# Kernel optimization log

Hardware: AMD Instinct MI355X
Metric: run time of the kernel (lower is better)

The kernel has to match this reference:

```python
import jax, jax.numpy as jnp
import numpy as np

T, OBS, H, NOBJ = 32768, 256, 512, 4


def _xavier(key, shape):
    fan_in, fan_out = shape[0], shape[1]
    lim = jnp.sqrt(6.0 / (fan_in + fan_out)).astype(jnp.float32)
    return jax.random.uniform(key, shape, jnp.float32, -lim, lim)


def setup_inputs() -> dict:
    key = jax.random.key(0)
    ks = jax.random.split(key, 16)
    # weights stored as [in, out] so y = x @ W (same math as nn.Linear with W.T)
    return {
        "x": jax.random.normal(ks[0], (T, OBS), jnp.float32),
        "W_in0": _xavier(ks[1], (OBS, H)),
        "W_B0": _xavier(ks[2], (OBS, H)),
        "W_C0": _xavier(ks[3], (OBS, H)),
        "W_d0": _xavier(ks[4], (OBS, H)),
        "A_log0": jax.random.normal(ks[5], (H,), jnp.float32),
        "W_in1": _xavier(ks[6], (H, H)),
        "W_B1": _xavier(ks[7], (H, H)),
        "W_C1": _xavier(ks[8], (H, H)),
        "W_d1": _xavier(ks[9], (H, H)),
        "A_log1": jax.random.normal(ks[10], (H,), jnp.float32),
        "W_out": _xavier(ks[11], (H, NOBJ)),
        "b_out": jnp.zeros((NOBJ,), jnp.float32),
        "W_skip": _xavier(ks[12], (OBS, NOBJ)),
    }


def _mamba_layer(x, W_in, W_B, W_C, W_d, A_log):
    # x: [T, D_in] -> [T, H]
    x_state = x @ W_in           # [T, H]
    B = x @ W_B                  # [T, H]
    C = x @ W_C                  # [T, H]
    delta = jax.nn.sigmoid(x @ W_d)  # [T, H]
    A = -jnp.exp(A_log)          # [H]
    A_bar = jnp.exp(delta * A)   # [T, H], in (0, 1)
    Bx = B * x_state             # [T, H]

    def step(h, inp):
        a_t, bx_t = inp
        h = a_t * h + bx_t
        return h, h

    h0 = jnp.zeros((x_state.shape[-1],), x_state.dtype)
    _, h_seq = jax.lax.scan(step, h0, (A_bar, Bx))  # [T, H]
    return C * h_seq


def reference(x, W_in0, W_B0, W_C0, W_d0, A_log0,
              W_in1, W_B1, W_C1, W_d1, A_log1,
              W_out, b_out, W_skip):
    skip = x
    y = _mamba_layer(x, W_in0, W_B0, W_C0, W_d0, A_log0)
    y = _mamba_layer(y, W_in1, W_B1, W_C1, W_d1, A_log1)
    out = y @ W_out + b_out + skip @ W_skip  # [T, NOBJ]
    return out
```

## Files before the change

kernel.cpp:

```cpp
#include <hip/hip_runtime.h>

typedef __attribute__((ext_vector_type(8))) short short8;
typedef __attribute__((ext_vector_type(4))) float floatx4;

#define T_SIZE 32768
#define OBS    256
#define H      512
#define NC     512
#define CHUNK  64
#define NGRP   32
#define GCH    16
#define SLAB   ((size_t)T_SIZE * 32)

__device__ __forceinline__ unsigned short f2bf(float f){
    union { float f; unsigned u; } v; v.f = f;
    unsigned u = v.u;
    u += 0x7FFFu + ((u >> 16) & 1u);
    return (unsigned short)(u >> 16);
}
__device__ __forceinline__ float bf2f(unsigned short u){
    union { unsigned u; float f; } v; v.u = ((unsigned)u) << 16; return v.f;
}

#define GLOAD_LDS16(g, l) \
    __builtin_amdgcn_global_load_lds((const __attribute__((address_space(1))) unsigned*)(g), \
                                     (__attribute__((address_space(3))) unsigned*)(l), 16, 0, 0)

__global__ void cast_x_kernel(const float* __restrict__ x, unsigned short* __restrict__ xb, int n4){
    int i = blockIdx.x * 256 + threadIdx.x;
    if (i < n4){
        float4 v = ((const float4*)x)[i];
        ushort4 o;
        o.x = f2bf(v.x); o.y = f2bf(v.y); o.z = f2bf(v.z); o.w = f2bf(v.w);
        ((ushort4*)xb)[i] = o;
    }
}

__global__ void tcast4_kernel(const float* __restrict__ W0, const float* __restrict__ W1,
                              const float* __restrict__ W2, const float* __restrict__ W3,
                              unsigned short* __restrict__ dst, int K, int KH){
    int idx = blockIdx.x * 256 + threadIdx.x;
    if (idx >= 4 * KH) return;
    int s   = idx / KH;
    int rem = idx - s * KH;
    int k = rem >> 9;
    int h = rem & 511;
    const float* W = (s == 0) ? W0 : (s == 1) ? W1 : (s == 2) ? W2 : W3;
    int b = h >> 4, hh = h & 15;
    dst[(size_t)((b * 4 + s) * 16 + hh) * K + k] = f2bf(W[(size_t)k * H + h]);
}

__global__ __launch_bounds__(256) void gemm_layer_kernel(
    const unsigned short* __restrict__ xb,
    const unsigned short* __restrict__ wt,
    const float* __restrict__ A_log,
    float* __restrict__ aT, unsigned short* __restrict__ bxT, unsigned short* __restrict__ CT,
    float* __restrict__ Pbuf, float* __restrict__ Hbuf,
    int K)
{
    __shared__ unsigned short SM[2][8192];

    const int tid  = threadIdx.x;
    const int wave = tid >> 6;
    const int lane = tid & 63;
    const int ml   = lane & 15;
    const int quad = lane >> 4;
    const int wm   = wave & 1;
    const int wn   = wave >> 1;

    const int flat = blockIdx.y * 16 + blockIdx.x;
    const int xcd  = flat & 7;
    const int j    = flat >> 3;
    const int nb   = j & 15;
    const int mb   = (j >> 4) * 8 + xcd;
    const int m0   = mb * 128;

    const int srow = tid >> 2;
    const int sel  = (((tid & 3) ^ ((tid >> 3) & 3))) * 8;
    const int swz  = (ml >> 1) & 3;

    const unsigned short* pa0 = xb + (size_t)(m0 + srow) * K + sel;
    const unsigned short* pa1 = pa0 + (size_t)64 * K;
    const unsigned short* pb0 = wt + (size_t)(nb * 128 + srow) * K + sel;
    const unsigned short* pb1 = pb0 + (size_t)64 * K;

    const int ldsA0 = (wave * 64 + 0  ) * 8;
    const int ldsA1 = (wave * 64 + 256) * 8;

    floatx4 acc[4][4];
    #pragma unroll
    for (int i = 0; i < 4; i++)
        #pragma unroll
        for (int jj = 0; jj < 4; jj++)
            acc[i][jj] = (floatx4)(0.0f);

    GLOAD_LDS16(pa0, &SM[0][ldsA0]);
    GLOAD_LDS16(pa1, &SM[0][ldsA1]);
    GLOAD_LDS16(pb0, &SM[0][4096 + ldsA0]);
    GLOAD_LDS16(pb1, &SM[0][4096 + ldsA1]);

    const int nk = K >> 5;
    for (int kk = 0; kk < nk; ++kk){
        __syncthreads();
        const int cur = kk & 1;
        if (kk + 1 < nk){
            const int nxt = cur ^ 1;
            const int ko  = (kk + 1) * 32;
            GLOAD_LDS16(pa0 + ko, &SM[nxt][ldsA0]);
            GLOAD_LDS16(pa1 + ko, &SM[nxt][ldsA1]);
            GLOAD_LDS16(pb0 + ko, &SM[nxt][4096 + ldsA0]);
            GLOAD_LDS16(pb1 + ko, &SM[nxt][4096 + ldsA1]);
        }

        const unsigned short* As = &SM[cur][0];
        const unsigned short* Bs = &SM[cur][4096];
        short8 av[4], bv[4];
        #pragma unroll
        for (int i = 0; i < 4; i++)
            av[i] = *(const short8*)(As + (size_t)(wm * 64 + i * 16 + ml) * 32 + (quad ^ swz) * 8);
        #pragma unroll
        for (int jj = 0; jj < 4; jj++)
            bv[jj] = *(const short8*)(Bs + (size_t)(wn * 64 + jj * 16 + ml) * 32 + (quad ^ swz) * 8);

        #pragma unroll
        for (int i = 0; i < 4; i++)
            #pragma unroll
            for (int jj = 0; jj < 4; jj++)
                acc[i][jj] = __builtin_amdgcn_mfma_f32_16x16x32_bf16(av[i], bv[jj], acc[i][jj], 0, 0, 0);
    }
    __syncthreads();

    unsigned short* SMe = &SM[0][0];
    const int col = wn * 16 + ml;
    const int h   = nb * 32 + col;
    const float Aneg = -expf(A_log[h]);

    float segp[4], segh[4];

    float* smf = (float*)SMe;
    #pragma unroll
    for (int i = 0; i < 4; i++){
        float p = 1.0f, hh = 0.0f;
        #pragma unroll
        for (int r = 0; r < 4; r++){
            int trow = wm * 64 + i * 16 + quad * 4 + r;
            float dv = acc[i][3][r];
            float delta = 1.0f / (1.0f + expf(-dv));
            float a  = expf(delta * Aneg);
            float bx = acc[i][1][r] * acc[i][0][r];
            smf[trow * 32 + col] = a;
            hh = fmaf(a, hh, bx);
            p *= a;
        }
        segp[i] = p; segh[i] = hh;
    }
    __syncthreads();
    {
        const float4* src = (const float4*)smf;
        float4* dst = (float4*)(aT + (size_t)nb * SLAB + (size_t)m0 * 32);
        #pragma unroll
        for (int v = 0; v < 4; v++) dst[tid + v * 256] = src[tid + v * 256];
    }
    __syncthreads();

    #pragma unroll
    for (int i = 0; i < 4; i++){
        #pragma unroll
        for (int r = 0; r < 4; r++){
            int trow = wm * 64 + i * 16 + quad * 4 + r;
            SMe[trow * 32 + col]        = f2bf(acc[i][1][r] * acc[i][0][r]);
            SMe[4096 + trow * 32 + col] = f2bf(acc[i][2][r]);
        }
    }
    __syncthreads();
    {
        const short8* s8 = (const short8*)SMe;
        short8* db = (short8*)(bxT + (size_t)nb * SLAB + (size_t)m0 * 32);
        short8* dc = (short8*)(CT  + (size_t)nb * SLAB + (size_t)m0 * 32);
        db[tid] = s8[tid];       db[tid + 256] = s8[tid + 256];
        dc[tid] = s8[512 + tid]; dc[tid + 256] = s8[768 + tid];
    }
    __syncthreads();

    float2* segbuf = (float2*)SMe;
    #pragma unroll
    for (int i = 0; i < 4; i++)
        segbuf[(i * 4 + quad) * 64 + col * 2 + wm] = make_float2(segp[i], segh[i]);
    __syncthreads();
    if (tid < 64){
        int ccol = tid >> 1, ch = tid & 1;
        float P = 1.0f, Hc = 0.0f;
        #pragma unroll
        for (int s = 0; s < 16; s++){
            float2 ph = segbuf[s * 64 + ccol * 2 + ch];
            Hc = fmaf(ph.x, Hc, ph.y);
            P *= ph.x;
        }
        int c = mb * 2 + ch;
        Pbuf[(size_t)c * H + nb * 32 + ccol] = P;
        Hbuf[(size_t)c * H + nb * 32 + ccol] = Hc;
    }
}

__global__ void scan2a_kernel(const float* __restrict__ P, const float* __restrict__ Hc,
                              float* __restrict__ Sloc, float* __restrict__ Pp,
                              float* __restrict__ Pg, float* __restrict__ Hg){
    const int g  = blockIdx.x;
    const int j4 = threadIdx.x * 4;
    float4 pc = {1.f,1.f,1.f,1.f}, hc = {0.f,0.f,0.f,0.f};
    #pragma unroll
    for (int i = 0; i < GCH; i++){
        size_t o = (size_t)(g * GCH + i) * H + j4;
        float4 P4 = *(const float4*)(P + o);
        float4 H4 = *(const float4*)(Hc + o);
        *(float4*)(Sloc + o) = hc;
        *(float4*)(Pp   + o) = pc;
        hc.x = fmaf(P4.x, hc.x, H4.x); pc.x *= P4.x;
        hc.y = fmaf(P4.y, hc.y, H4.y); pc.y *= P4.y;
        hc.z = fmaf(P4.z, hc.z, H4.z); pc.z *= P4.z;
        hc.w = fmaf(P4.w, hc.w, H4.w); pc.w *= P4.w;
    }
    *(float4*)(Pg + (size_t)g * H + j4) = pc;
    *(float4*)(Hg + (size_t)g * H + j4) = hc;
}

__global__ void scan2b_kernel(const float* __restrict__ Pg, const float* __restrict__ Hg,
                              float* __restrict__ Cg){
    const int j = threadIdx.x;
    float carry = 0.0f;
    for (int g0 = 0; g0 < NGRP; g0 += 8){
        float p[8], h[8];
        #pragma unroll
        for (int i = 0; i < 8; i++){
            p[i] = Pg[(size_t)(g0 + i) * H + j];
            h[i] = Hg[(size_t)(g0 + i) * H + j];
        }
        #pragma unroll
        for (int i = 0; i < 8; i++){
            Cg[(size_t)(g0 + i) * H + j] = carry;
            carry = fmaf(p[i], carry, h[i]);
        }
    }
}

__global__ void scan3_bf16_kernel(const float* __restrict__ aT, const unsigned short* __restrict__ bxT,
                                  const unsigned short* __restrict__ CT,
                                  const float* __restrict__ Sloc, const float* __restrict__ Pp,
                                  const float* __restrict__ Cg,
                                  unsigned short* __restrict__ yb){
    int idx = blockIdx.x * 256 + threadIdx.x;
    int j4 = (idx & 127) * 4;
    int c  = idx >> 7;
    int nb = j4 >> 5, jj = j4 & 31;
    size_t so = (size_t)c * H + j4;
    size_t go = (size_t)(c >> 4) * H + j4;
    float4 sl = *(const float4*)(Sloc + so);
    float4 pp = *(const float4*)(Pp + so);
    float4 cg = *(const float4*)(Cg + go);
    float4 h;
    h.x = fmaf(pp.x, cg.x, sl.x);
    h.y = fmaf(pp.y, cg.y, sl.y);
    h.z = fmaf(pp.z, cg.z, sl.z);
    h.w = fmaf(pp.w, cg.w, sl.w);
    size_t off = (size_t)nb * SLAB + (size_t)c * CHUNK * 32 + jj;
    size_t yo  = (size_t)c * CHUNK * H + j4;
    #pragma unroll 4
    for (int i = 0; i < CHUNK; i++){
        float4 av  = *(const float4*)(aT + off);
        ushort4 bv = *(const ushort4*)(bxT + off);
        ushort4 cv = *(const ushort4*)(CT + off);
        h.x = fmaf(av.x, h.x, bf2f(bv.x));
        h.y = fmaf(av.y, h.y, bf2f(bv.y));
        h.z = fmaf(av.z, h.z, bf2f(bv.z));
        h.w = fmaf(av.w, h.w, bf2f(bv.w));
        ushort4 o;
        o.x = f2bf(bf2f(cv.x) * h.x);
        o.y = f2bf(bf2f(cv.y) * h.y);
        o.z = f2bf(bf2f(cv.z) * h.z);
        o.w = f2bf(bf2f(cv.w) * h.w);
        *(ushort4*)(yb + yo) = o;
        off += 32; yo += H;
    }
}

__global__ __launch_bounds__(256) void final_kernel(const unsigned short* __restrict__ y2,
                                                    const float* __restrict__ x,
                                                    const float* __restrict__ Wout,
                                                    const float* __restrict__ bout,
                                                    const float* __restrict__ Wskip,
                                                    float* __restrict__ out){
    int wave = threadIdx.x >> 6;
    int lane = threadIdx.x & 63;
    int t = blockIdx.x * 4 + wave;
    float s0 = 0.f, s1 = 0.f, s2 = 0.f, s3 = 0.f;
    const float4* W4 = (const float4*)Wout;
    #pragma unroll
    for (int k = lane; k < H; k += 64){
        float yv = bf2f(y2[(size_t)t * H + k]);
        float4 w = W4[k];
        s0 = fmaf(yv, w.x, s0); s1 = fmaf(yv, w.y, s1);
        s2 = fmaf(yv, w.z, s2); s3 = fmaf(yv, w.w, s3);
    }
    const float4* S4 = (const float4*)Wskip;
    #pragma unroll
    for (int k = lane; k < OBS; k += 64){
        float xv = x[(size_t)t * OBS + k];
        float4 w = S4[k];
        s0 = fmaf(xv, w.x, s0); s1 = fmaf(xv, w.y, s1);
        s2 = fmaf(xv, w.z, s2); s3 = fmaf(xv, w.w, s3);
    }
    #pragma unroll
    for (int off = 32; off > 0; off >>= 1){
        s0 += __shfl_down(s0, off);
        s1 += __shfl_down(s1, off);
        s2 += __shfl_down(s2, off);
        s3 += __shfl_down(s3, off);
    }
    if (lane == 0){
        out[(size_t)t * 4 + 0] = s0 + bout[0];
        out[(size_t)t * 4 + 1] = s1 + bout[1];
        out[(size_t)t * 4 + 2] = s2 + bout[2];
        out[(size_t)t * 4 + 3] = s3 + bout[3];
    }
}

extern "C" void kernel_launch(void* const* d_in, const int* in_sizes, int n_in,
                              void* d_out, int out_size, void* d_ws, size_t ws_size,
                              hipStream_t stream)
{
    const float* x     = (const float*)d_in[0];
    const float* W_in0 = (const float*)d_in[1];
    const float* W_B0  = (const float*)d_in[2];
    const float* W_C0  = (const float*)d_in[3];
    const float* W_d0  = (const float*)d_in[4];
    const float* A0    = (const float*)d_in[5];
    const float* W_in1 = (const float*)d_in[6];
    const float* W_B1  = (const float*)d_in[7];
    const float* W_C1  = (const float*)d_in[8];
    const float* W_d1  = (const float*)d_in[9];
    const float* A1    = (const float*)d_in[10];
    const float* Wout  = (const float*)d_in[11];
    const float* bout  = (const float*)d_in[12];
    const float* Wskip = (const float*)d_in[13];
    float* out = (float*)d_out;

    char* ws = (char*)d_ws;
    size_t off = 0;
    auto alloc = [&](size_t bytes) -> void* {
        void* p = ws + off;
        off += (bytes + 255) & ~(size_t)255;
        return p;
    };
    unsigned short* xb  = (unsigned short*)alloc((size_t)T_SIZE * OBS * 2);
    unsigned short* yb  = (unsigned short*)alloc((size_t)T_SIZE * H * 2);
    unsigned short* Wt0 = (unsigned short*)alloc((size_t)4 * H * OBS * 2);
    unsigned short* Wt1 = (unsigned short*)alloc((size_t)4 * H * H * 2);
    float*          aT  = (float*)alloc((size_t)T_SIZE * H * 4);
    unsigned short* bxT = (unsigned short*)alloc((size_t)T_SIZE * H * 2);
    unsigned short* CT  = (unsigned short*)alloc((size_t)T_SIZE * H * 2);
    float* Pbuf = (float*)alloc((size_t)NC * H * 4);
    float* Hbuf = (float*)alloc((size_t)NC * H * 4);
    float* Sloc = (float*)alloc((size_t)NC * H * 4);
    float* Pp   = (float*)alloc((size_t)NC * H * 4);
    float* Pg   = (float*)alloc((size_t)NGRP * H * 4);
    float* Hg   = (float*)alloc((size_t)NGRP * H * 4);
    float* Cg   = (float*)alloc((size_t)NGRP * H * 4);
    (void)ws_size; (void)in_sizes; (void)n_in; (void)out_size;

    cast_x_kernel<<<(T_SIZE * OBS / 4 + 255) / 256, 256, 0, stream>>>(x, xb, T_SIZE * OBS / 4);
    tcast4_kernel<<<(4 * OBS * H + 255) / 256, 256, 0, stream>>>(W_in0, W_B0, W_C0, W_d0, Wt0, OBS, OBS * H);
    tcast4_kernel<<<(4 * H   * H + 255) / 256, 256, 0, stream>>>(W_in1, W_B1, W_C1, W_d1, Wt1, H,   H * H);

    dim3 ggrid(16, 256);
    const int sgrid = NC * 128 / 256;

    gemm_layer_kernel<<<ggrid, 256, 0, stream>>>(xb, Wt0, A0, aT, bxT, CT, Pbuf, Hbuf, OBS);
    scan2a_kernel<<<NGRP, 128, 0, stream>>>(Pbuf, Hbuf, Sloc, Pp, Pg, Hg);
    scan2b_kernel<<<1, H, 0, stream>>>(Pg, Hg, Cg);
    scan3_bf16_kernel<<<sgrid, 256, 0, stream>>>(aT, bxT, CT, Sloc, Pp, Cg, yb);

    gemm_layer_kernel<<<ggrid, 256, 0, stream>>>(yb, Wt1, A1, aT, bxT, CT, Pbuf, Hbuf, H);
    scan2a_kernel<<<NGRP, 128, 0, stream>>>(Pbuf, Hbuf, Sloc, Pp, Pg, Hg);
    scan2b_kernel<<<1, H, 0, stream>>>(Pg, Hg, Cg);
    scan3_bf16_kernel<<<sgrid, 256, 0, stream>>>(aT, bxT, CT, Sloc, Pp, Cg, yb );

    final_kernel<<<T_SIZE / 4, 256, 0, stream>>>(yb, x, Wout, bout, Wskip, out);
}
```

Before: 366.6 us.

## Store bf16 log-decay instead of fp32 decay and drop scan prefix buffers

The GEMM epilogue now writes the log-decay delta*A as bf16 instead of the fp32 exp value, and scan3 recomputes exp per element, which halves the decay stream's traffic. The Sloc/Pp intermediate buffers are removed: groups shrink to 8 chunks and scan3 reconstructs each chunk's start state by replaying up to 7 prior chunk summaries. The final kernel reads the bf16 copy of x instead of the fp32 one. This trades memory bandwidth for extra exp work and short serial loops, and adds bf16 rounding error to the decay and the skip path.

```diff
diff --git a/kernel.cpp b/kernel.cpp
--- a/kernel.cpp
+++ b/kernel.cpp
@@ -8,8 +8,8 @@
 #define H      512
 #define NC     512
 #define CHUNK  64
-#define NGRP   32
-#define GCH    16
+#define NGRP   64
+#define GCH    8
 #define SLAB   ((size_t)T_SIZE * 32)
 
 __device__ __forceinline__ unsigned short f2bf(float f){
@@ -54,7 +54,7 @@
     const unsigned short* __restrict__ xb,
     const unsigned short* __restrict__ wt,
     const float* __restrict__ A_log,
-    float* __restrict__ aT, unsigned short* __restrict__ bxT, unsigned short* __restrict__ CT,
+    unsigned short* __restrict__ gT, unsigned short* __restrict__ bxT, unsigned short* __restrict__ CT,
     float* __restrict__ Pbuf, float* __restrict__ Hbuf,
     int K)
 {
@@ -136,8 +136,6 @@
     const float Aneg = -expf(A_log[h]);
 
     float segp[4], segh[4];
-
-    float* smf = (float*)SMe;
     #pragma unroll
     for (int i = 0; i < 4; i++){
         float p = 1.0f, hh = 0.0f;
@@ -146,39 +144,26 @@
             int trow = wm * 64 + i * 16 + quad * 4 + r;
             float dv = acc[i][3][r];
             float delta = 1.0f / (1.0f + expf(-dv));
-            float a  = expf(delta * Aneg);
-            float bx = acc[i][1][r] * acc[i][0][r];
-            smf[trow * 32 + col] = a;
-            hh = fmaf(a, hh, bx);
+            unsigned short gb = f2bf(delta * Aneg);
+            float a = expf(bf2f(gb));
+            unsigned short bb = f2bf(acc[i][1][r] * acc[i][0][r]);
+            SMe[        trow * 32 + col] = gb;
+            SMe[4096 +  trow * 32 + col] = bb;
+            SMe[8192 +  trow * 32 + col] = f2bf(acc[i][2][r]);
+            hh = fmaf(a, hh, bf2f(bb));
             p *= a;
         }
         segp[i] = p; segh[i] = hh;
-    }
-    __syncthreads();
-    {
-        const float4* src = (const float4*)smf;
-        float4* dst = (float4*)(aT + (size_t)nb * SLAB + (size_t)m0 * 32);
-        #pragma unroll
-        for (int v = 0; v < 4; v++) dst[tid + v * 256] = src[tid + v * 256];
-    }
-    __syncthreads();
-
-    #pragma unroll
-    for (int i = 0; i < 4; i++){
-        #pragma unroll
-        for (int r = 0; r < 4; r++){
-            int trow = wm * 64 + i * 16 + quad * 4 + r;
-            SMe[trow * 32 + col]        = f2bf(acc[i][1][r] * acc[i][0][r]);
-            SMe[4096 + trow * 32 + col] = f2bf(acc[i][2][r]);
-        }
     }
     __syncthreads();
     {
         const short8* s8 = (const short8*)SMe;
+        short8* dg = (short8*)(gT  + (size_t)nb * SLAB + (size_t)m0 * 32);
         short8* db = (short8*)(bxT + (size_t)nb * SLAB + (size_t)m0 * 32);
         short8* dc = (short8*)(CT  + (size_t)nb * SLAB + (size_t)m0 * 32);
-        db[tid] = s8[tid];       db[tid + 256] = s8[tid + 256];
-        dc[tid] = s8[512 + tid]; dc[tid + 256] = s8[768 + tid];
+        dg[tid] = s8[tid];        dg[tid + 256] = s8[tid + 256];
+        db[tid] = s8[512 + tid];  db[tid + 256] = s8[768 + tid];
+        dc[tid] = s8[1024 + tid]; dc[tid + 256] = s8[1280 + tid];
     }
     __syncthreads();
 
@@ -203,7 +188,6 @@
 }
 
 __global__ void scan2a_kernel(const float* __restrict__ P, const float* __restrict__ Hc,
-                              float* __restrict__ Sloc, float* __restrict__ Pp,
                               float* __restrict__ Pg, float* __restrict__ Hg){
     const int g  = blockIdx.x;
     const int j4 = threadIdx.x * 4;
@@ -213,8 +197,6 @@
         size_t o = (size_t)(g * GCH + i) * H + j4;
         float4 P4 = *(const float4*)(P + o);
         float4 H4 = *(const float4*)(Hc + o);
-        *(float4*)(Sloc + o) = hc;
-        *(float4*)(Pp   + o) = pc;
         hc.x = fmaf(P4.x, hc.x, H4.x); pc.x *= P4.x;
         hc.y = fmaf(P4.y, hc.y, H4.y); pc.y *= P4.y;
         hc.z = fmaf(P4.z, hc.z, H4.z); pc.z *= P4.z;
@@ -243,36 +225,36 @@
     }
 }
 
-__global__ void scan3_bf16_kernel(const float* __restrict__ aT, const unsigned short* __restrict__ bxT,
-                                  const unsigned short* __restrict__ CT,
-                                  const float* __restrict__ Sloc, const float* __restrict__ Pp,
-                                  const float* __restrict__ Cg,
-                                  unsigned short* __restrict__ yb){
+__global__ void scan3_kernel(const unsigned short* __restrict__ gT, const unsigned short* __restrict__ bxT,
+                             const unsigned short* __restrict__ CT,
+                             const float* __restrict__ P, const float* __restrict__ Hc,
+                             const float* __restrict__ Cg,
+                             unsigned short* __restrict__ yb){
     int idx = blockIdx.x * 256 + threadIdx.x;
     int j4 = (idx & 127) * 4;
     int c  = idx >> 7;
     int nb = j4 >> 5, jj = j4 & 31;
-    size_t so = (size_t)c * H + j4;
-    size_t go = (size_t)(c >> 4) * H + j4;
-    float4 sl = *(const float4*)(Sloc + so);
-    float4 pp = *(const float4*)(Pp + so);
-    float4 cg = *(const float4*)(Cg + go);
-    float4 h;
-    h.x = fmaf(pp.x, cg.x, sl.x);
-    h.y = fmaf(pp.y, cg.y, sl.y);
-    h.z = fmaf(pp.z, cg.z, sl.z);
-    h.w = fmaf(pp.w, cg.w, sl.w);
+    int grp = c >> 3;
+    float4 h = *(const float4*)(Cg + (size_t)grp * H + j4);
+    for (int cc = grp << 3; cc < c; ++cc){
+        float4 P4 = *(const float4*)(P + (size_t)cc * H + j4);
+        float4 H4 = *(const float4*)(Hc + (size_t)cc * H + j4);
+        h.x = fmaf(P4.x, h.x, H4.x);
+        h.y = fmaf(P4.y, h.y, H4.y);
+        h.z = fmaf(P4.z, h.z, H4.z);
+        h.w = fmaf(P4.w, h.w, H4.w);
+    }
     size_t off = (size_t)nb * SLAB + (size_t)c * CHUNK * 32 + jj;
     size_t yo  = (size_t)c * CHUNK * H + j4;
-    #pragma unroll 4
+    #pragma unroll 8
     for (int i = 0; i < CHUNK; i++){
-        float4 av  = *(const float4*)(aT + off);
+        ushort4 gv = *(const ushort4*)(gT + off);
         ushort4 bv = *(const ushort4*)(bxT + off);
         ushort4 cv = *(const ushort4*)(CT + off);
-        h.x = fmaf(av.x, h.x, bf2f(bv.x));
-        h.y = fmaf(av.y, h.y, bf2f(bv.y));
-        h.z = fmaf(av.z, h.z, bf2f(bv.z));
-        h.w = fmaf(av.w, h.w, bf2f(bv.w));
+        h.x = fmaf(expf(bf2f(gv.x)), h.x, bf2f(bv.x));
+        h.y = fmaf(expf(bf2f(gv.y)), h.y, bf2f(bv.y));
+        h.z = fmaf(expf(bf2f(gv.z)), h.z, bf2f(bv.z));
+        h.w = fmaf(expf(bf2f(gv.w)), h.w, bf2f(bv.w));
         ushort4 o;
         o.x = f2bf(bf2f(cv.x) * h.x);
         o.y = f2bf(bf2f(cv.y) * h.y);
@@ -284,7 +266,7 @@
 }
 
 __global__ __launch_bounds__(256) void final_kernel(const unsigned short* __restrict__ y2,
-                                                    const float* __restrict__ x,
+                                                    const unsigned short* __restrict__ xb,
                                                     const float* __restrict__ Wout,
                                                     const float* __restrict__ bout,
                                                     const float* __restrict__ Wskip,
@@ -304,7 +286,7 @@
     const float4* S4 = (const float4*)Wskip;
     #pragma unroll
     for (int k = lane; k < OBS; k += 64){
-        float xv = x[(size_t)t * OBS + k];
+        float xv = bf2f(xb[(size_t)t * OBS + k]);
         float4 w = S4[k];
         s0 = fmaf(xv, w.x, s0); s1 = fmaf(xv, w.y, s1);
         s2 = fmaf(xv, w.z, s2); s3 = fmaf(xv, w.w, s3);
@@ -355,13 +337,11 @@
     unsigned short* yb  = (unsigned short*)alloc((size_t)T_SIZE * H * 2);
     unsigned short* Wt0 = (unsigned short*)alloc((size_t)4 * H * OBS * 2);
     unsigned short* Wt1 = (unsigned short*)alloc((size_t)4 * H * H * 2);
-    float*          aT  = (float*)alloc((size_t)T_SIZE * H * 4);
+    unsigned short* gT  = (unsigned short*)alloc((size_t)T_SIZE * H * 2);
     unsigned short* bxT = (unsigned short*)alloc((size_t)T_SIZE * H * 2);
     unsigned short* CT  = (unsigned short*)alloc((size_t)T_SIZE * H * 2);
     float* Pbuf = (float*)alloc((size_t)NC * H * 4);
     float* Hbuf = (float*)alloc((size_t)NC * H * 4);
-    float* Sloc = (float*)alloc((size_t)NC * H * 4);
-    float* Pp   = (float*)alloc((size_t)NC * H * 4);
     float* Pg   = (float*)alloc((size_t)NGRP * H * 4);
     float* Hg   = (float*)alloc((size_t)NGRP * H * 4);
     float* Cg   = (float*)alloc((size_t)NGRP * H * 4);
@@ -374,15 +354,15 @@
     dim3 ggrid(16, 256);
     const int sgrid = NC * 128 / 256;
 
-    gemm_layer_kernel<<<ggrid, 256, 0, stream>>>(xb, Wt0, A0, aT, bxT, CT, Pbuf, Hbuf, OBS);
-    scan2a_kernel<<<NGRP, 128, 0, stream>>>(Pbuf, Hbuf, Sloc, Pp, Pg, Hg);
+    gemm_layer_kernel<<<ggrid, 256, 0, stream>>>(xb, Wt0, A0, gT, bxT, CT, Pbuf, Hbuf, OBS);
+    scan2a_kernel<<<NGRP, 128, 0, stream>>>(Pbuf, Hbuf, Pg, Hg);
     scan2b_kernel<<<1, H, 0, stream>>>(Pg, Hg, Cg);
-    scan3_bf16_kernel<<<sgrid, 256, 0, stream>>>(aT, bxT, CT, Sloc, Pp, Cg, yb);
-
-    gemm_layer_kernel<<<ggrid, 256, 0, stream>>>(yb, Wt1, A1, aT, bxT, CT, Pbuf, Hbuf, H);
-    scan2a_kernel<<<NGRP, 128, 0, stream>>>(Pbuf, Hbuf, Sloc, Pp, Pg, Hg);
+    scan3_kernel<<<sgrid, 256, 0, stream>>>(gT, bxT, CT, Pbuf, Hbuf, Cg, yb);
+
+    gemm_layer_kernel<<<ggrid, 256, 0, stream>>>(yb, Wt1, A1, gT, bxT, CT, Pbuf, Hbuf, H);
+    scan2a_kernel<<<NGRP, 128, 0, stream>>>(Pbuf, Hbuf, Pg, Hg);
     scan2b_kernel<<<1, H, 0, stream>>>(Pg, Hg, Cg);
-    scan3_bf16_kernel<<<sgrid, 256, 0, stream>>>(aT, bxT, CT, Sloc, Pp, Cg, yb );
-
-    final_kernel<<<T_SIZE / 4, 256, 0, stream>>>(yb, x, Wout, bout, Wskip, out);
-}
+    scan3_kernel<<<sgrid, 256, 0, stream>>>(gT, bxT, CT, Pbuf, Hbuf, Cg, yb );
+
+    final_kernel<<<T_SIZE / 4, 256, 0, stream>>>(yb, xb, Wout, bout, Wskip, out);
+}
```

Result: faster. 347.6 us (-5.2%).
